# Performance work log

Hardware: AMD Instinct MI355X
Metric: run time of the kernel (lower is better)

The kernel has to match this reference:

```python
import jax, jax.numpy as jnp
import numpy as np

BN_EPS = 1e-5


def setup_inputs() -> dict:
    key = jax.random.key(0)
    ks = jax.random.split(key, 13)
    B, C, H, W = 8, 256, 96, 32
    D = C // 2  # inter_channels
    s = 0.05
    return {
        "x": jax.random.normal(ks[0], (B, C, H, W), jnp.float32),
        "g_w": jax.random.normal(ks[1], (D, C), jnp.float32) * s,
        "g_b": jax.random.normal(ks[2], (D,), jnp.float32) * s,
        "theta_w": jax.random.normal(ks[3], (D, C), jnp.float32) * s,
        "theta_b": jax.random.normal(ks[4], (D,), jnp.float32) * s,
        "phi_w": jax.random.normal(ks[5], (D, C), jnp.float32) * s,
        "phi_b": jax.random.normal(ks[6], (D,), jnp.float32) * s,
        "w_w": jax.random.normal(ks[7], (C, D), jnp.float32) * s,
        "w_b": jax.random.normal(ks[8], (C,), jnp.float32) * s,
        "bn_gamma": jax.random.normal(ks[9], (C,), jnp.float32),
        "bn_beta": jax.random.normal(ks[10], (C,), jnp.float32) * s,
        "bn_mean": jax.random.normal(ks[11], (C,), jnp.float32) * s,
        "bn_var": jax.random.uniform(ks[12], (C,), jnp.float32),
    }


def reference(x, g_w, g_b, theta_w, theta_b, phi_w, phi_b, w_w, w_b,
              bn_gamma, bn_beta, bn_mean, bn_var):
    B, C, H, W = x.shape
    N = H * W
    xf = x.reshape(B, C, N)  # flatten spatial: (B, C, N)

    # 1x1 conv projections == per-pixel linear maps
    g_x = jnp.einsum('dc,bcn->bnd', g_w, xf) + g_b            # (B, N, D)
    theta_x = jnp.einsum('dc,bcn->bnd', theta_w, xf) + theta_b  # (B, N, D)
    phi_x = jnp.einsum('dc,bcn->bdn', phi_w, xf) + phi_b[:, None]  # (B, D, N)

    # unnormalized attention: f = theta phi^T / N, then y = f g
    f_div_C = jnp.einsum('bnd,bdm->bnm', theta_x, phi_x) / N  # (B, N, N)
    y = jnp.einsum('bnm,bmd->bnd', f_div_C, g_x)              # (B, N, D)

    # output 1x1 conv + eval-mode BatchNorm2d
    wy = jnp.einsum('cd,bnd->bcn', w_w, y) + w_b[:, None]     # (B, C, N)
    inv = bn_gamma / jnp.sqrt(bn_var + BN_EPS)
    wy = (wy - bn_mean[:, None]) * inv[:, None] + bn_beta[:, None]

    z = wy.reshape(B, C, H, W) + x  # residual
    return z
```

## Files before the change

### kernel.cpp

```cpp
#include <hip/hip_runtime.h>
#include <hip/hip_bf16.h>
#include <cstddef>

typedef __attribute__((ext_vector_type(8))) short short8;
typedef __attribute__((ext_vector_type(4))) float floatx4;
typedef __hip_bfloat16 bf16;

#define NB 8
#define NC 256
#define ND 128
#define NN 3072
#define BN_EPS 1e-5f

static __device__ __forceinline__ short f2s(float v) {
    bf16 h = __float2bfloat16(v);
    return *reinterpret_cast<short*>(&h);
}

__global__ __launch_bounds__(256) void setup_kernel(
    const float* __restrict__ phi_w, const float* __restrict__ g_w,
    const float* __restrict__ theta_w, short* __restrict__ Wall)
{
    int t = threadIdx.x;
    int r = blockIdx.x;
    const float* src = (r < 128) ? (phi_w + (size_t)r * NC)
                     : (r < 256) ? (g_w + (size_t)(r - 128) * NC)
                                 : (theta_w + (size_t)(r - 256) * NC);
    Wall[(size_t)r * NC + t] = f2s(src[t]);
}

__global__ __launch_bounds__(384)
void proj_kernel(const float* __restrict__ x, const short* __restrict__ Wall,
                 const float* __restrict__ phi_b, const float* __restrict__ g_b,
                 const float* __restrict__ theta_b,
                 short* __restrict__ thDN, float* __restrict__ Mbuf)
{
    __shared__ short PGs[256][72];
    __shared__ short Xs[64][72];
    int b = blockIdx.y;
    int n0 = blockIdx.x * 64;
    int t = threadIdx.x;
    int lane = t & 63;
    int wave = t >> 6;
    int lm = lane & 15;
    int lk = (lane >> 4) * 8;

    const float* xb = x + (size_t)b * NC * NN;

    floatx4 zero = {0.f, 0.f, 0.f, 0.f};
    floatx4 acc[4][4];
#pragma unroll
    for (int i = 0; i < 4; ++i)
#pragma unroll
        for (int j = 0; j < 4; ++j) acc[i][j] = zero;

#pragma unroll
    for (int kt = 0; kt < NC; kt += 64) {
        __syncthreads();
        if (t < 256) {
            int sn = t & 63, cg = t >> 6;
            const float* src = xb + (size_t)(kt + cg * 16) * NN + n0 + sn;
            short8 s0, s1;
#pragma unroll
            for (int j = 0; j < 8; ++j) {
                s0[j] = f2s(src[(size_t)j * NN]);
                s1[j] = f2s(src[(size_t)(8 + j) * NN]);
            }
            *(short8*)&Xs[sn][cg * 16]     = s0;
            *(short8*)&Xs[sn][cg * 16 + 8] = s1;
        }
        __syncthreads();
#pragma unroll
        for (int kk = 0; kk < 64; kk += 32) {
            short8 af[4], bfr[4];
#pragma unroll
            for (int i = 0; i < 4; ++i)
                af[i] = *(const short8*)(Wall +
                        (size_t)(wave * 64 + i * 16 + lm) * NC + kt + kk + lk);
#pragma unroll
            for (int j = 0; j < 4; ++j)
                bfr[j] = *(const short8*)&Xs[j * 16 + lm][kk + lk];
#pragma unroll
            for (int i = 0; i < 4; ++i)
#pragma unroll
                for (int j = 0; j < 4; ++j)
                    acc[i][j] = __builtin_amdgcn_mfma_f32_16x16x32_bf16(
                        af[i], bfr[j], acc[i][j], 0, 0, 0);
        }
    }

    int row0 = wave * 64 + (lane >> 4) * 4;

    if (wave < 4) {
#pragma unroll
        for (int i = 0; i < 4; ++i) {
#pragma unroll
            for (int r = 0; r < 4; ++r) {
                int row = row0 + i * 16 + r;
                float bv = (row < 128) ? phi_b[row] : g_b[row - 128];
#pragma unroll
                for (int j = 0; j < 4; ++j)
                    PGs[row][lm + j * 16] = f2s(acc[i][j][r] + bv);
            }
        }
    } else {
        short* Tb = thDN + (size_t)b * ND * NN;
#pragma unroll
        for (int i = 0; i < 4; ++i) {
#pragma unroll
            for (int r = 0; r < 4; ++r) {
                int d = row0 - 256 + i * 16 + r;
                float bv = theta_b[d];
#pragma unroll
                for (int j = 0; j < 4; ++j)
                    Tb[(size_t)d * NN + n0 + lm + j * 16] =
                        f2s(acc[i][j][r] + bv);
            }
        }
    }
    __syncthreads();

    if (wave < 4) {
        int wr = wave >> 1, wc = wave & 1;
        floatx4 macc[4][4];
#pragma unroll
        for (int i = 0; i < 4; ++i)
#pragma unroll
            for (int j = 0; j < 4; ++j) macc[i][j] = zero;
#pragma unroll
        for (int kk = 0; kk < 64; kk += 32) {
            short8 af[4], bfr[4];
#pragma unroll
            for (int i = 0; i < 4; ++i)
                af[i] = *(const short8*)&PGs[wr * 64 + i * 16 + lm][kk + lk];
#pragma unroll
            for (int j = 0; j < 4; ++j)
                bfr[j] = *(const short8*)&PGs[128 + wc * 64 + j * 16 + lm][kk + lk];
#pragma unroll
            for (int i = 0; i < 4; ++i)
#pragma unroll
                for (int j = 0; j < 4; ++j)
                    macc[i][j] = __builtin_amdgcn_mfma_f32_16x16x32_bf16(
                        af[i], bfr[j], macc[i][j], 0, 0, 0);
        }
        float* Mf = Mbuf + (size_t)b * ND * ND;
        int mr0 = wr * 64 + (lane >> 4) * 4;
        int mc0 = wc * 64 + lm;
        const float sc = 1.f / (float)NN;
#pragma unroll
        for (int i = 0; i < 4; ++i)
#pragma unroll
            for (int j = 0; j < 4; ++j)
#pragma unroll
                for (int r = 0; r < 4; ++r)
                    atomicAdd(&Mf[(size_t)(mr0 + i * 16 + r) * ND + mc0 + j * 16],
                              macc[i][j][r] * sc);
    }
}

__global__ __launch_bounds__(256)
void final_kernel(const float* __restrict__ Mbuf, const short* __restrict__ thDN,
                  const float* __restrict__ w_w, const float* __restrict__ w_b,
                  const float* __restrict__ gamma, const float* __restrict__ beta,
                  const float* __restrict__ mean, const float* __restrict__ var,
                  const float* __restrict__ x, float* __restrict__ out)
{
    __shared__ short As[128][72];
    __shared__ short Bs[128][72];
    __shared__ short P2s[128][136];
    int b = blockIdx.z;
    int tile_m = blockIdx.y * 128;
    int tile_n = blockIdx.x * 128;
    int t = threadIdx.x;
    int lane = t & 63;
    int wave = t >> 6;
    int wr = wave >> 1, wc = wave & 1;
    int lm = lane & 15;
    int lk = (lane >> 4) * 8;
    int ch = (t & 7) * 8;
    int r0 = t >> 3;

    const float* Mb = Mbuf + (size_t)b * ND * ND;

    floatx4 zero = {0.f, 0.f, 0.f, 0.f};
    floatx4 acc[4][4];
#pragma unroll
    for (int i = 0; i < 4; ++i)
#pragma unroll
        for (int j = 0; j < 4; ++j) acc[i][j] = zero;

#pragma unroll
    for (int kt = 0; kt < ND; kt += 64) {
        __syncthreads();
#pragma unroll
        for (int p = 0; p < 4; ++p) {
            int r = r0 + p * 32;
            const float* ap = w_w + (size_t)(tile_m + r) * ND + kt + ch;
            const float* bp = Mb + (size_t)r * ND + kt + ch;
            floatx4 a0 = *(const floatx4*)ap, a1 = *(const floatx4*)(ap + 4);
            floatx4 b0 = *(const floatx4*)bp, b1 = *(const floatx4*)(bp + 4);
            short8 sa, sb;
#pragma unroll
            for (int j = 0; j < 4; ++j) {
                sa[j] = f2s(a0[j]); sa[4 + j] = f2s(a1[j]);
                sb[j] = f2s(b0[j]); sb[4 + j] = f2s(b1[j]);
            }
            *(short8*)&As[r][ch] = sa;
            *(short8*)&Bs[r][ch] = sb;
        }
        __syncthreads();
#pragma unroll
        for (int kk = 0; kk < 64; kk += 32) {
            short8 af[4], bfr[4];
#pragma unroll
            for (int i = 0; i < 4; ++i)
                af[i] = *(const short8*)&As[wr * 64 + i * 16 + lm][kk + lk];
#pragma unroll
            for (int j = 0; j < 4; ++j)
                bfr[j] = *(const short8*)&Bs[wc * 64 + j * 16 + lm][kk + lk];
#pragma unroll
            for (int i = 0; i < 4; ++i)
#pragma unroll
                for (int j = 0; j < 4; ++j)
                    acc[i][j] = __builtin_amdgcn_mfma_f32_16x16x32_bf16(
                        af[i], bfr[j], acc[i][j], 0, 0, 0);
        }
    }

    {
        int row0 = wr * 64 + (lane >> 4) * 4;
        int col0 = wc * 64 + lm;
#pragma unroll
        for (int i = 0; i < 4; ++i) {
#pragma unroll
            for (int r = 0; r < 4; ++r) {
                int cl = row0 + i * 16 + r;
                int c = tile_m + cl;
                float iv = gamma[c] * rsqrtf(var[c] + BN_EPS);
#pragma unroll
                for (int j = 0; j < 4; ++j)
                    P2s[cl][col0 + j * 16] = f2s(acc[i][j][r] * iv);
            }
        }
    }

    floatx4 acc2[4][4];
#pragma unroll
    for (int i = 0; i < 4; ++i)
#pragma unroll
        for (int j = 0; j < 4; ++j) acc2[i][j] = zero;

    const short* Tb = thDN + (size_t)b * ND * NN;
#pragma unroll
    for (int kt = 0; kt < ND; kt += 64) {
        __syncthreads();
        {
            int dl = t & 63;
            int ng = t >> 6;
            const short* src = Tb + (size_t)(kt + dl) * NN + tile_n + ng * 32;
#pragma unroll
            for (int q = 0; q < 4; ++q) {
                short8 v = *(const short8*)(src + q * 8);
#pragma unroll
                for (int jj = 0; jj < 8; ++jj)
                    Bs[ng * 32 + q * 8 + jj][dl] = v[jj];
            }
        }
        __syncthreads();
#pragma unroll
        for (int kk = 0; kk < 64; kk += 32) {
            short8 af[4], bfr[4];
#pragma unroll
            for (int i = 0; i < 4; ++i)
                af[i] = *(const short8*)&P2s[wr * 64 + i * 16 + lm][kt + kk + lk];
#pragma unroll
            for (int j = 0; j < 4; ++j)
                bfr[j] = *(const short8*)&Bs[wc * 64 + j * 16 + lm][kk + lk];
#pragma unroll
            for (int i = 0; i < 4; ++i)
#pragma unroll
                for (int j = 0; j < 4; ++j)
                    acc2[i][j] = __builtin_amdgcn_mfma_f32_16x16x32_bf16(
                        af[i], bfr[j], acc2[i][j], 0, 0, 0);
        }
    }

    int crow0 = tile_m + wr * 64 + (lane >> 4) * 4;
    int col0 = tile_n + wc * 64 + lm;
    float* Cf = out + (size_t)b * NC * NN;
    const float* Rg = x + (size_t)b * NC * NN;
#pragma unroll
    for (int i = 0; i < 4; ++i) {
#pragma unroll
        for (int r = 0; r < 4; ++r) {
            int c = crow0 + i * 16 + r;
            float iv = gamma[c] * rsqrtf(var[c] + BN_EPS);
            float b2 = iv * (w_b[c] - mean[c]) + beta[c];
#pragma unroll
            for (int j = 0; j < 4; ++j) {
                size_t idx = (size_t)c * NN + col0 + j * 16;
                Cf[idx] = acc2[i][j][r] + b2 + Rg[idx];
            }
        }
    }
}

extern "C" void kernel_launch(void* const* d_in, const int* in_sizes, int n_in,
                              void* d_out, int out_size, void* d_ws, size_t ws_size,
                              hipStream_t stream)
{
    const float* x       = (const float*)d_in[0];
    const float* g_w     = (const float*)d_in[1];
    const float* g_b     = (const float*)d_in[2];
    const float* theta_w = (const float*)d_in[3];
    const float* theta_b = (const float*)d_in[4];
    const float* phi_w   = (const float*)d_in[5];
    const float* phi_b   = (const float*)d_in[6];
    const float* w_w     = (const float*)d_in[7];
    const float* w_b     = (const float*)d_in[8];
    const float* gamma   = (const float*)d_in[9];
    const float* beta    = (const float*)d_in[10];
    const float* mean    = (const float*)d_in[11];
    const float* var     = (const float*)d_in[12];
    (void)in_sizes; (void)n_in; (void)out_size; (void)ws_size;

    char* w = (char*)d_ws;
    short* thDN = (short*)w; w += (size_t)NB * ND * NN * 2;
    float* Mbuf = (float*)w; w += (size_t)NB * ND * ND * 4;
    short* Wall = (short*)w; w += (size_t)384 * NC * 2;

    setup_kernel<<<dim3(384), dim3(256), 0, stream>>>(
        phi_w, g_w, theta_w, Wall);

    proj_kernel<<<dim3(NN / 64, NB), dim3(384), 0, stream>>>(
        x, Wall, phi_b, g_b, theta_b, thDN, Mbuf);

    final_kernel<<<dim3(NN / 128, NC / 128, NB), 256, 0, stream>>>(
        Mbuf, thDN, w_w, w_b, gamma, beta, mean, var, x, (float*)d_out);
}
```

Baseline: 160.0 us.

## Replace atomic accumulation of M with per-block partials and a reduce kernel

```diff
diff --git a/kernel.cpp b/kernel.cpp
--- a/kernel.cpp
+++ b/kernel.cpp
@@ -10,6 +10,7 @@
 #define NC 256
 #define ND 128
 #define NN 3072
+#define NBLK 48
 #define BN_EPS 1e-5f
 
 static __device__ __forceinline__ short f2s(float v) {
@@ -33,7 +34,7 @@
 void proj_kernel(const float* __restrict__ x, const short* __restrict__ Wall,
                  const float* __restrict__ phi_b, const float* __restrict__ g_b,
                  const float* __restrict__ theta_b,
-                 short* __restrict__ thDN, float* __restrict__ Mbuf)
+                 short* __restrict__ thDN, float* __restrict__ Mpart)
 {
     __shared__ short PGs[256][72];
     __shared__ short Xs[64][72];
@@ -143,7 +144,7 @@
                     macc[i][j] = __builtin_amdgcn_mfma_f32_16x16x32_bf16(
                         af[i], bfr[j], macc[i][j], 0, 0, 0);
         }
-        float* Mf = Mbuf + (size_t)b * ND * ND;
+        float* Mf = Mpart + ((size_t)b * NBLK + blockIdx.x) * (ND * ND);
         int mr0 = wr * 64 + (lane >> 4) * 4;
         int mc0 = wc * 64 + lm;
         const float sc = 1.f / (float)NN;
@@ -153,13 +154,26 @@
             for (int j = 0; j < 4; ++j)
 #pragma unroll
                 for (int r = 0; r < 4; ++r)
-                    atomicAdd(&Mf[(size_t)(mr0 + i * 16 + r) * ND + mc0 + j * 16],
-                              macc[i][j][r] * sc);
+                    Mf[(size_t)(mr0 + i * 16 + r) * ND + mc0 + j * 16] =
+                        macc[i][j][r] * sc;
     }
 }
 
 __global__ __launch_bounds__(256)
-void final_kernel(const float* __restrict__ Mbuf, const short* __restrict__ thDN,
+void reduce_kernel(const float* __restrict__ Mpart, short* __restrict__ Mb16)
+{
+    int idx = blockIdx.x * 256 + threadIdx.x;
+    int b = idx >> 14;
+    int e = idx & 16383;
+    const float* src = Mpart + (size_t)b * NBLK * 16384 + e;
+    float s = 0.f;
+#pragma unroll 8
+    for (int p = 0; p < NBLK; ++p) s += src[(size_t)p * 16384];
+    Mb16[(size_t)b * 16384 + e] = f2s(s);
+}
+
+__global__ __launch_bounds__(256)
+void final_kernel(const short* __restrict__ Mb16, const short* __restrict__ thDN,
                   const float* __restrict__ w_w, const float* __restrict__ w_b,
                   const float* __restrict__ gamma, const float* __restrict__ beta,
                   const float* __restrict__ mean, const float* __restrict__ var,
@@ -180,7 +194,7 @@
     int ch = (t & 7) * 8;
     int r0 = t >> 3;
 
-    const float* Mb = Mbuf + (size_t)b * ND * ND;
+    const short* Mb = Mb16 + (size_t)b * ND * ND;
 
     floatx4 zero = {0.f, 0.f, 0.f, 0.f};
     floatx4 acc[4][4];
@@ -196,17 +210,12 @@
         for (int p = 0; p < 4; ++p) {
             int r = r0 + p * 32;
             const float* ap = w_w + (size_t)(tile_m + r) * ND + kt + ch;
-            const float* bp = Mb + (size_t)r * ND + kt + ch;
             floatx4 a0 = *(const floatx4*)ap, a1 = *(const floatx4*)(ap + 4);
-            floatx4 b0 = *(const floatx4*)bp, b1 = *(const floatx4*)(bp + 4);
-            short8 sa, sb;
-#pragma unroll
-            for (int j = 0; j < 4; ++j) {
-                sa[j] = f2s(a0[j]); sa[4 + j] = f2s(a1[j]);
-                sb[j] = f2s(b0[j]); sb[4 + j] = f2s(b1[j]);
-            }
+            short8 sa;
+#pragma unroll
+            for (int j = 0; j < 4; ++j) { sa[j] = f2s(a0[j]); sa[4 + j] = f2s(a1[j]); }
             *(short8*)&As[r][ch] = sa;
-            *(short8*)&Bs[r][ch] = sb;
+            *(short8*)&Bs[r][ch] = *(const short8*)(Mb + (size_t)r * ND + kt + ch);
         }
         __syncthreads();
 #pragma unroll
@@ -325,16 +334,19 @@
     (void)in_sizes; (void)n_in; (void)out_size; (void)ws_size;
 
     char* w = (char*)d_ws;
-    short* thDN = (short*)w; w += (size_t)NB * ND * NN * 2;
-    float* Mbuf = (float*)w; w += (size_t)NB * ND * ND * 4;
-    short* Wall = (short*)w; w += (size_t)384 * NC * 2;
+    short* thDN  = (short*)w; w += (size_t)NB * ND * NN * 2;
+    float* Mpart = (float*)w; w += (size_t)NB * NBLK * ND * ND * 4;
+    short* Mb16  = (short*)w; w += (size_t)NB * ND * ND * 2;
+    short* Wall  = (short*)w; w += (size_t)384 * NC * 2;
 
     setup_kernel<<<dim3(384), dim3(256), 0, stream>>>(
         phi_w, g_w, theta_w, Wall);
 
     proj_kernel<<<dim3(NN / 64, NB), dim3(384), 0, stream>>>(
-        x, Wall, phi_b, g_b, theta_b, thDN, Mbuf);
+        x, Wall, phi_b, g_b, theta_b, thDN, Mpart);
+
+    reduce_kernel<<<dim3(512), dim3(256), 0, stream>>>(Mpart, Mb16);
 
     final_kernel<<<dim3(NN / 128, NC / 128, NB), 256, 0, stream>>>(
-        Mbuf, thDN, w_w, w_b, gamma, beta, mean, var, x, (float*)d_out);
-}
+        Mb16, thDN, w_w, w_b, gamma, beta, mean, var, x, (float*)d_out);
+}
```

After: 135.8 us. -15.1%, faster.
